# Kernel optimization log

Hardware: AMD Instinct MI355X
Metric: run time of the kernel (lower is better)

The kernel has to match this reference:

```python
import jax, jax.numpy as jnp
import numpy as np

D_MODEL = 1024
NUM_HEADS = 16
D_K = D_MODEL // NUM_HEADS


def setup_inputs() -> dict:
    key = jax.random.key(0)
    ks = jax.random.split(key, 9)
    B, S = 4, 2048
    scale = 1.0 / np.sqrt(D_MODEL)
    x = jax.random.normal(ks[0], (B, S, D_MODEL), dtype=jnp.float32)
    wq = jax.random.normal(ks[1], (D_MODEL, D_MODEL), dtype=jnp.float32) * scale
    wk = jax.random.normal(ks[2], (D_MODEL, D_MODEL), dtype=jnp.float32) * scale
    wv = jax.random.normal(ks[3], (D_MODEL, D_MODEL), dtype=jnp.float32) * scale
    wo = jax.random.normal(ks[4], (D_MODEL, D_MODEL), dtype=jnp.float32) * scale
    bq = jax.random.normal(ks[5], (D_MODEL,), dtype=jnp.float32) * 0.01
    bk = jax.random.normal(ks[6], (D_MODEL,), dtype=jnp.float32) * 0.01
    bv = jax.random.normal(ks[7], (D_MODEL,), dtype=jnp.float32) * 0.01
    bo = jax.random.normal(ks[8], (D_MODEL,), dtype=jnp.float32) * 0.01
    return {"x": x, "wq": wq, "bq": bq, "wk": wk, "bk": bk,
            "wv": wv, "bv": bv, "wo": wo, "bo": bo}


def reference(x, wq, bq, wk, bk, wv, bv, wo, bo):
    B, S, _ = x.shape
    # projections -> [B, H, S, d_k]
    def split_heads(t):
        return t.reshape(B, S, NUM_HEADS, D_K).transpose(0, 2, 1, 3)
    q = split_heads(x @ wq.T + bq)
    k = split_heads(x @ wk.T + bk)
    v = split_heads(x @ wv.T + bv)
    scores = jnp.einsum("bhqd,bhkd->bhqk", q, k) / np.sqrt(D_K).astype(np.float32)
    attn = jax.nn.softmax(scores, axis=-1)  # dropout is identity at eval
    out = jnp.einsum("bhqk,bhkd->bhqd", attn, v)
    out = out.transpose(0, 2, 1, 3).reshape(B, S, D_MODEL)
    return out @ wo.T + bo
```

## Files before the change

kernel.cpp:

```cpp
#include <hip/hip_runtime.h>

#define D_MODEL 1024
#define NHEADS  16
#define DK      64
#define BATCH   4
#define SEQ     2048
#define MROWS   (BATCH*SEQ)
#define BHCOUNT (BATCH*NHEADS)
#define KTILES  (SEQ/64)

typedef _Float16 half8 __attribute__((ext_vector_type(8)));
typedef _Float16 half4 __attribute__((ext_vector_type(4)));
typedef float    floatx4 __attribute__((ext_vector_type(4)));
typedef float    floatx16 __attribute__((ext_vector_type(16)));

__device__ __forceinline__ void load_lds16(const void* g, void* l) {
    __builtin_amdgcn_global_load_lds((const __attribute__((address_space(1))) void*)g,
                                     (__attribute__((address_space(3))) void*)l, 16, 0, 0);
}

__device__ __forceinline__ unsigned pkrtz_u32(float a, float b) {
    auto h = __builtin_amdgcn_cvt_pkrtz(a, b);
    union { decltype(h) v; unsigned u; } c; c.v = h; return c.u;
}

__device__ __forceinline__ int permrow(int r) {
    return (r & ~12) | ((r & 4) << 1) | ((r & 8) >> 1);
}

__global__ __launch_bounds__(256)
void cvt_f32_f16(const float* __restrict__ in, _Float16* __restrict__ out) {
    size_t i = ((size_t)blockIdx.x*256 + threadIdx.x)*4;
    float4 v = *(const float4*)(in + i);
    half4 h = {(_Float16)v.x, (_Float16)v.y, (_Float16)v.z, (_Float16)v.w};
    *(half4*)(out + i) = h;
}

__global__ __launch_bounds__(256)
void cvt4_f32_f16(const float* __restrict__ a, const float* __restrict__ b,
                  const float* __restrict__ c, const float* __restrict__ d,
                  _Float16* __restrict__ oa, _Float16* __restrict__ ob,
                  _Float16* __restrict__ oc, _Float16* __restrict__ od) {
    const float* src; _Float16* dst;
    switch (blockIdx.y) {
        case 0:  src=a; dst=oa; break;
        case 1:  src=b; dst=ob; break;
        case 2:  src=c; dst=oc; break;
        default: src=d; dst=od; break;
    }
    size_t i = ((size_t)blockIdx.x*256 + threadIdx.x)*4;
    float4 v = *(const float4*)(src + i);
    half4 h = {(_Float16)v.x, (_Float16)v.y, (_Float16)v.z, (_Float16)v.w};
    *(half4*)(dst + i) = h;
}

template<int MODE>
__global__ __launch_bounds__(256)
void gemm_nt_f16(const _Float16* __restrict__ A, const _Float16* __restrict__ W,
                 const float* __restrict__ bias, void* __restrict__ Cout, float scale)
{
    __shared__ _Float16 As[2][128*64];
    __shared__ _Float16 Ws[2][128*64];
    const int t = threadIdx.x;
    const int w = t >> 6, l = t & 63;
    const int wm = w >> 1, wn = w & 1;

    const int L   = blockIdx.x + (int)gridDim.x * blockIdx.y;
    const int cpx = (int)(gridDim.x * gridDim.y) >> 3;
    const int wid = (L & 7) * cpx + (L >> 3);
    const int bn  = (wid & 7) * 128;
    const int bm  = (wid >> 3) * 128;

    const int lrow = l & 15, lq4 = l >> 4;

    int srow[4], scol[4];
    #pragma unroll
    for (int it = 0; it < 4; ++it) {
        int s = (it*4 + w)*64 + l;
        int r = s >> 3;
        srow[it] = r;
        scol[it] = ((s & 7) ^ (r & 7))*8;
    }

    floatx4 acc[4][4];
    #pragma unroll
    for (int i = 0; i < 4; ++i)
        #pragma unroll
        for (int j = 0; j < 4; ++j) acc[i][j] = (floatx4){0.f,0.f,0.f,0.f};

    #pragma unroll
    for (int it = 0; it < 4; ++it) {
        load_lds16(A + (size_t)(bm + srow[it])*1024 + scol[it], &As[0][((it*4+w)*64+l)*8]);
        load_lds16(W + (size_t)(bn + srow[it])*1024 + scol[it], &Ws[0][((it*4+w)*64+l)*8]);
    }

    for (int kt = 0; kt < 16; ++kt) {
        __syncthreads();
        const int cur = kt & 1;
        if (kt + 1 < 16) {
            const int k1 = (kt + 1)*64;
            #pragma unroll
            for (int it = 0; it < 4; ++it) {
                load_lds16(A + (size_t)(bm + srow[it])*1024 + k1 + scol[it], &As[cur^1][((it*4+w)*64+l)*8]);
                load_lds16(W + (size_t)(bn + srow[it])*1024 + k1 + scol[it], &Ws[cur^1][((it*4+w)*64+l)*8]);
            }
        }
        #pragma unroll
        for (int ks = 0; ks < 2; ++ks) {
            const int xg = (((ks*4) ^ lq4 ^ (lrow & 7)))*8;
            half8 af[4], bf[4];
            #pragma unroll
            for (int i = 0; i < 4; ++i) af[i] = *(half8*)&As[cur][(wm*64 + i*16 + lrow)*64 + xg];
            #pragma unroll
            for (int j = 0; j < 4; ++j) bf[j] = *(half8*)&Ws[cur][(wn*64 + j*16 + lrow)*64 + xg];
            __builtin_amdgcn_s_setprio(1);
            #pragma unroll
            for (int i = 0; i < 4; ++i)
                #pragma unroll
                for (int j = 0; j < 4; ++j)
                    acc[i][j] = __builtin_amdgcn_mfma_f32_16x16x32_f16(af[i], bf[j], acc[i][j], 0, 0, 0);
            __builtin_amdgcn_s_setprio(0);
        }
    }

    #pragma unroll
    for (int j = 0; j < 4; ++j) {
        int gcol = bn + wn*64 + j*16 + lrow;
        float bv = bias[gcol];
        #pragma unroll
        for (int i = 0; i < 4; ++i) {
            #pragma unroll
            for (int r = 0; r < 4; ++r) {
                int gm = bm + wm*64 + i*16 + lq4*4 + r;
                float val = (acc[i][j][r] + bv) * scale;
                if (MODE == 0) {
                    ((float*)Cout)[(size_t)gm*1024 + gcol] = val;
                } else {
                    int b = gm >> 11, s = gm & 2047;
                    int h = gcol >> 6, dk = gcol & 63;
                    ((_Float16*)Cout)[(((size_t)(b*NHEADS + h))*SEQ + s)*DK + dk] = (_Float16)val;
                }
            }
        }
    }
}

__global__ __launch_bounds__(256)
void transpose_v(const _Float16* __restrict__ V, _Float16* __restrict__ Vt)
{
    __shared__ unsigned Lt[64][33];
    const int t = threadIdx.x;
    const int bh = blockIdx.y;
    const int s0 = blockIdx.x*64;
    const _Float16* Vb = V + ((size_t)bh*SEQ + s0)*DK;
    const int sp = t >> 3, dkc = (t & 7)*8;
    uint4 r0 = *(const uint4*)(Vb + (2*sp+0)*64 + dkc);
    uint4 r1 = *(const uint4*)(Vb + (2*sp+1)*64 + dkc);
    unsigned a0[4] = {r0.x, r0.y, r0.z, r0.w};
    unsigned a1[4] = {r1.x, r1.y, r1.z, r1.w};
    #pragma unroll
    for (int i = 0; i < 4; ++i) {
        Lt[dkc+2*i+0][sp] = (a0[i] & 0xFFFFu) | (a1[i] << 16);
        Lt[dkc+2*i+1][sp] = (a0[i] >> 16)     | (a1[i] & 0xFFFF0000u);
    }
    __syncthreads();
    const int dk = t >> 2, spc = (t & 3)*8;
    uint4 o0 = {Lt[dk][spc+0], Lt[dk][spc+1], Lt[dk][spc+2], Lt[dk][spc+3]};
    uint4 o1 = {Lt[dk][spc+4], Lt[dk][spc+5], Lt[dk][spc+6], Lt[dk][spc+7]};
    _Float16* dst = Vt + ((size_t)bh*DK + dk)*SEQ + s0 + spc*2;
    *(uint4*)(dst)     = o0;
    *(uint4*)(dst + 8) = o1;
}

__global__ __launch_bounds__(128)
void attn_mfma(const _Float16* __restrict__ Q, const _Float16* __restrict__ K,
               const _Float16* __restrict__ Vt, _Float16* __restrict__ AO)
{
    __shared__ _Float16 Ks[2][64*64];
    __shared__ _Float16 Vs[2][64*64];

    const int t = threadIdx.x;
    const int w = t >> 6, l = t & 63;
    const int l31 = l & 31, hi = l >> 5;

    const int L   = blockIdx.x + (int)gridDim.x * blockIdx.y;
    const int wid = (L & 7) * 128 + (L >> 3);
    const int bh  = wid >> 4;
    const int q0  = (wid & 15) * 128;

    const _Float16* Qb = Q  + ((size_t)bh*SEQ + q0)*DK;
    const _Float16* Kb = K  + (size_t)bh*SEQ*DK;
    const _Float16* Vb = Vt + (size_t)bh*DK*SEQ;

    int srow[4], scol[4], karow[4];
    #pragma unroll
    for (int it = 0; it < 4; ++it) {
        int s = (it*2 + w)*64 + l;
        int r = s >> 3;
        int lc = (s & 7) ^ (r & 7);
        srow[it] = r; scol[it] = lc*8;
        karow[it] = permrow(r);
    }

    half8 qf[2][4];
    #pragma unroll
    for (int qt = 0; qt < 2; ++qt)
        #pragma unroll
        for (int kk = 0; kk < 4; ++kk)
            qf[qt][kk] = *(const half8*)(Qb + (size_t)(w*64 + qt*32 + l31)*DK + kk*16 + hi*8);

    #pragma unroll
    for (int it = 0; it < 4; ++it) {
        load_lds16(Kb + (size_t)karow[it]*DK + scol[it], &Ks[0][(it*2+w)*512]);
        load_lds16(Vb + (size_t)srow[it]*SEQ + scol[it], &Vs[0][(it*2+w)*512]);
    }

    floatx16 Oacc[2][2];
    floatx16 lacc[2];
    #pragma unroll
    for (int qt = 0; qt < 2; ++qt) {
        #pragma unroll
        for (int i = 0; i < 16; ++i) { Oacc[qt][0][i] = 0.f; Oacc[qt][1][i] = 0.f; lacc[qt][i] = 0.f; }
    }
    floatx16 z16;
    #pragma unroll
    for (int i = 0; i < 16; ++i) z16[i] = 0.f;
    half8 onesf;
    #pragma unroll
    for (int i = 0; i < 8; ++i) onesf[i] = (_Float16)1.f;

#define ATTN_PREFETCH(NBUF, KT1)                                                          \
    if ((KT1) < KTILES) {                                                                 \
        _Pragma("unroll")                                                                 \
        for (int it = 0; it < 4; ++it) {                                                  \
            load_lds16(Kb + ((size_t)((KT1)*64 + karow[it]))*DK + scol[it],               \
                       &Ks[NBUF][(it*2+w)*512]);                                          \
            load_lds16(Vb + (size_t)srow[it]*SEQ + (KT1)*64 + scol[it],                   \
                       &Vs[NBUF][(it*2+w)*512]);                                          \
        }                                                                                 \
    }

#define ATTN_STEP(CUR, KT)                                                                \
    {                                                                                     \
        __syncthreads();                                                                  \
        ATTN_PREFETCH((CUR)^1, (KT)+1)                                                    \
        _Pragma("unroll")                                                                 \
        for (int kb = 0; kb < 2; ++kb) {                                                  \
            const int row = kb*32 + l31;                                                  \
                                \
            floatx16 sTa, sTb;                                                            \
            {                                                                             \
                half8 kf = *(half8*)&Ks[CUR][row*64 + ((hi ^ (row & 7)))*8];              \
                sTa = __builtin_amdgcn_mfma_f32_32x32x16_f16(kf, qf[0][0], z16, 0, 0, 0); \
                sTb = __builtin_amdgcn_mfma_f32_32x32x16_f16(kf, qf[1][0], z16, 0, 0, 0); \
            }                                                                             \
            _Pragma("unroll")                                                             \
            for (int kk = 1; kk < 4; ++kk) {                                              \
                half8 kf = *(half8*)&Ks[CUR][row*64 + (((kk*2 + hi) ^ (row & 7)))*8];     \
                sTa = __builtin_amdgcn_mfma_f32_32x32x16_f16(kf, qf[0][kk], sTa, 0, 0, 0);\
                sTb = __builtin_amdgcn_mfma_f32_32x32x16_f16(kf, qf[1][kk], sTb, 0, 0, 0);\
            }                                                                             \
                     \
            unsigned Wda[8], Wdb[8];                                                      \
            _Pragma("unroll")                                                             \
            for (int p = 0; p < 8; ++p) {                                                 \
                Wda[p] = pkrtz_u32(__builtin_amdgcn_exp2f(sTa[2*p]),                      \
                                   __builtin_amdgcn_exp2f(sTa[2*p+1]));                   \
                Wdb[p] = pkrtz_u32(__builtin_amdgcn_exp2f(sTb[2*p]),                      \
                                   __builtin_amdgcn_exp2f(sTb[2*p+1]));                   \
            }                                                                             \
                                     \
            _Pragma("unroll")                                                             \
            for (int kk2 = 0; kk2 < 2; ++kk2) {                                           \
                union { unsigned u[4]; half8 h; } pfa, pfb;                               \
                _Pragma("unroll")                                                         \
                for (int v = 0; v < 4; ++v) { pfa.u[v] = Wda[kk2*4 + v];                  \
                                              pfb.u[v] = Wdb[kk2*4 + v]; }                \
                lacc[0] = __builtin_amdgcn_mfma_f32_32x32x16_f16(pfa.h, onesf, lacc[0], 0, 0, 0); \
                lacc[1] = __builtin_amdgcn_mfma_f32_32x32x16_f16(pfb.h, onesf, lacc[1], 0, 0, 0); \
                const int vg = kb*4 + kk2*2 + hi;                                         \
                _Pragma("unroll")                                                         \
                for (int n = 0; n < 2; ++n) {                                             \
                    const int vrow = n*32 + l31;                                          \
                    half8 vf = *(half8*)&Vs[CUR][vrow*64 + ((vg ^ (vrow & 7)))*8];        \
                    Oacc[0][n] = __builtin_amdgcn_mfma_f32_32x32x16_f16(pfa.h, vf, Oacc[0][n], 0, 0, 0); \
                    Oacc[1][n] = __builtin_amdgcn_mfma_f32_32x32x16_f16(pfb.h, vf, Oacc[1][n], 0, 0, 0); \
                }                                                                         \
            }                                                                             \
        }                                                                                 \
    }

    for (int ktp = 0; ktp < KTILES; ktp += 2) {
        ATTN_STEP(0, ktp)
        ATTN_STEP(1, ktp+1)
    }
#undef ATTN_STEP
#undef ATTN_PREFETCH

    const int b = bh >> 4, h = bh & 15;
    #pragma unroll
    for (int qt = 0; qt < 2; ++qt)
        #pragma unroll
        for (int r = 0; r < 16; ++r) {
            float inv = 1.f / lacc[qt][r];
            int qrow = (r & 3) + 8*(r >> 2) + 4*hi;
            int gq = q0 + w*64 + qt*32 + qrow;
            _Float16* dst = AO + ((size_t)(b*SEQ + gq))*D_MODEL + h*DK;
            dst[l31]      = (_Float16)(Oacc[qt][0][r] * inv);
            dst[32 + l31] = (_Float16)(Oacc[qt][1][r] * inv);
        }
}

extern "C" void kernel_launch(void* const* d_in, const int* in_sizes, int n_in,
                              void* d_out, int out_size, void* d_ws, size_t ws_size,
                              hipStream_t stream)
{
    const float* x  = (const float*)d_in[0];
    const float* wq = (const float*)d_in[1];
    const float* bq = (const float*)d_in[2];
    const float* wk = (const float*)d_in[3];
    const float* bk = (const float*)d_in[4];
    const float* wv = (const float*)d_in[5];
    const float* bv = (const float*)d_in[6];
    const float* wo = (const float*)d_in[7];
    const float* bo = (const float*)d_in[8];

    const size_t NX = (size_t)MROWS * D_MODEL;
    const size_t NW = (size_t)D_MODEL * D_MODEL;
    _Float16* xh  = (_Float16*)d_ws;
    _Float16* wqh = xh  + NX;
    _Float16* wkh = wqh + NW;
    _Float16* wvh = wkh + NW;
    _Float16* woh = wvh + NW;
    _Float16* Qh  = woh + NW;
    _Float16* Kh  = Qh  + NX;
    _Float16* Vh  = Kh  + NX;
    _Float16* Vth = Vh  + NX;
    _Float16* AOh = Vth + NX;

    cvt_f32_f16<<<NX/1024, 256, 0, stream>>>(x, xh);
    cvt4_f32_f16<<<dim3(NW/1024, 4), 256, 0, stream>>>(wq, wk, wv, wo, wqh, wkh, wvh, woh);

    const float QSCALE = 0.125f * 1.44269504f;
    dim3 pgrid(D_MODEL/128, MROWS/128);
    gemm_nt_f16<1><<<pgrid, 256, 0, stream>>>(xh, wqh, bq, Qh, QSCALE);
    gemm_nt_f16<1><<<pgrid, 256, 0, stream>>>(xh, wkh, bk, Kh, 1.0f);
    gemm_nt_f16<1><<<pgrid, 256, 0, stream>>>(xh, wvh, bv, Vh, 1.0f);

    transpose_v<<<dim3(SEQ/64, BHCOUNT), 256, 0, stream>>>(Vh, Vth);
    attn_mfma<<<dim3(SEQ/128, BHCOUNT), 128, 0, stream>>>(Qh, Kh, Vth, AOh);

    gemm_nt_f16<0><<<pgrid, 256, 0, stream>>>(AOh, woh, bo, d_out, 1.0f);
}
```

Measured before the change: 299.4 us.

## Fuse Q/K/V projections into one GEMM launch with BK=32 tiles

The three separate Q, K and V projection GEMMs become a single launch over a 3x wider N grid. Contiguous wq/wk/wv half buffers act as one 3072x1024 weight, and each tile picks its bias, scale and output buffer from its column block. The GEMM is templated on the K tile depth with a matching LDS swizzle, and the fused launch uses BK=32 to halve shared memory per block and allow more resident blocks. The aim is to cut launch overhead and tail effects across three small grids, at the cost of more K iterations and barriers per tile.

New measurement: 300.0 us. No clear change (+0.2%).

```diff
diff --git a/kernel.cpp b/kernel.cpp
--- a/kernel.cpp
+++ b/kernel.cpp
@@ -54,32 +54,39 @@
     *(half4*)(dst + i) = h;
 }
 
-template<int MODE>
+template<int MODE, int BK>
 __global__ __launch_bounds__(256)
 void gemm_nt_f16(const _Float16* __restrict__ A, const _Float16* __restrict__ W,
-                 const float* __restrict__ bias, void* __restrict__ Cout, float scale)
+                 const float* __restrict__ b0, const float* __restrict__ b1,
+                 const float* __restrict__ b2, void* __restrict__ Cout, float qscale)
 {
-    __shared__ _Float16 As[2][128*64];
-    __shared__ _Float16 Ws[2][128*64];
+    constexpr int GR  = BK/8;
+    constexpr int NIT = BK/16;
+    constexpr int NKT = 1024/BK;
+    constexpr int KS  = BK/32;
+    __shared__ _Float16 As[2][128*BK];
+    __shared__ _Float16 Ws[2][128*BK];
     const int t = threadIdx.x;
     const int w = t >> 6, l = t & 63;
     const int wm = w >> 1, wn = w & 1;
 
     const int L   = blockIdx.x + (int)gridDim.x * blockIdx.y;
+    const int nbx = gridDim.x;
     const int cpx = (int)(gridDim.x * gridDim.y) >> 3;
     const int wid = (L & 7) * cpx + (L >> 3);
-    const int bn  = (wid & 7) * 128;
-    const int bm  = (wid >> 3) * 128;
+    const int bn  = (wid % nbx) * 128;
+    const int bm  = (wid / nbx) * 128;
 
     const int lrow = l & 15, lq4 = l >> 4;
 
-    int srow[4], scol[4];
-    #pragma unroll
-    for (int it = 0; it < 4; ++it) {
+    int srow[NIT], scol[NIT];
+    #pragma unroll
+    for (int it = 0; it < NIT; ++it) {
         int s = (it*4 + w)*64 + l;
-        int r = s >> 3;
-        srow[it] = r;
-        scol[it] = ((s & 7) ^ (r & 7))*8;
+        int r = s / GR, g = s % GR, gs;
+        if constexpr (BK == 64) gs = g ^ (r & 7);
+        else                    gs = g ^ ((r >> 1) & 3);
+        srow[it] = r; scol[it] = gs*8;
     }
 
     floatx4 acc[4][4];
@@ -89,30 +96,32 @@
         for (int j = 0; j < 4; ++j) acc[i][j] = (floatx4){0.f,0.f,0.f,0.f};
 
     #pragma unroll
-    for (int it = 0; it < 4; ++it) {
-        load_lds16(A + (size_t)(bm + srow[it])*1024 + scol[it], &As[0][((it*4+w)*64+l)*8]);
-        load_lds16(W + (size_t)(bn + srow[it])*1024 + scol[it], &Ws[0][((it*4+w)*64+l)*8]);
-    }
-
-    for (int kt = 0; kt < 16; ++kt) {
+    for (int it = 0; it < NIT; ++it) {
+        load_lds16(A + (size_t)(bm + srow[it])*1024 + scol[it], &As[0][(it*4+w)*512]);
+        load_lds16(W + (size_t)(bn + srow[it])*1024 + scol[it], &Ws[0][(it*4+w)*512]);
+    }
+
+    for (int kt = 0; kt < NKT; ++kt) {
         __syncthreads();
         const int cur = kt & 1;
-        if (kt + 1 < 16) {
-            const int k1 = (kt + 1)*64;
-            #pragma unroll
-            for (int it = 0; it < 4; ++it) {
-                load_lds16(A + (size_t)(bm + srow[it])*1024 + k1 + scol[it], &As[cur^1][((it*4+w)*64+l)*8]);
-                load_lds16(W + (size_t)(bn + srow[it])*1024 + k1 + scol[it], &Ws[cur^1][((it*4+w)*64+l)*8]);
+        if (kt + 1 < NKT) {
+            const int k1 = (kt + 1)*BK;
+            #pragma unroll
+            for (int it = 0; it < NIT; ++it) {
+                load_lds16(A + (size_t)(bm + srow[it])*1024 + k1 + scol[it], &As[cur^1][(it*4+w)*512]);
+                load_lds16(W + (size_t)(bn + srow[it])*1024 + k1 + scol[it], &Ws[cur^1][(it*4+w)*512]);
             }
         }
         #pragma unroll
-        for (int ks = 0; ks < 2; ++ks) {
-            const int xg = (((ks*4) ^ lq4 ^ (lrow & 7)))*8;
+        for (int ks = 0; ks < KS; ++ks) {
+            int xg;
+            if constexpr (BK == 64) xg = ((ks*4 + lq4) ^ (lrow & 7))*8;
+            else                    xg = (lq4 ^ ((lrow >> 1) & 3))*8;
             half8 af[4], bf[4];
             #pragma unroll
-            for (int i = 0; i < 4; ++i) af[i] = *(half8*)&As[cur][(wm*64 + i*16 + lrow)*64 + xg];
-            #pragma unroll
-            for (int j = 0; j < 4; ++j) bf[j] = *(half8*)&Ws[cur][(wn*64 + j*16 + lrow)*64 + xg];
+            for (int i = 0; i < 4; ++i) af[i] = *(half8*)&As[cur][(wm*64 + i*16 + lrow)*BK + xg];
+            #pragma unroll
+            for (int j = 0; j < 4; ++j) bf[j] = *(half8*)&Ws[cur][(wn*64 + j*16 + lrow)*BK + xg];
             __builtin_amdgcn_s_setprio(1);
             #pragma unroll
             for (int i = 0; i < 4; ++i)
@@ -123,10 +132,14 @@
         }
     }
 
+    constexpr size_t NXc = (size_t)MROWS * D_MODEL;
+    const int which = bn >> 10;
+    const float* bptr = (which == 0) ? b0 : (which == 1) ? b1 : b2;
+    const float scale = (which == 0) ? qscale : 1.0f;
     #pragma unroll
     for (int j = 0; j < 4; ++j) {
         int gcol = bn + wn*64 + j*16 + lrow;
-        float bv = bias[gcol];
+        float bv = bptr[gcol & 1023];
         #pragma unroll
         for (int i = 0; i < 4; ++i) {
             #pragma unroll
@@ -136,9 +149,10 @@
                 if (MODE == 0) {
                     ((float*)Cout)[(size_t)gm*1024 + gcol] = val;
                 } else {
+                    int hc = gcol & 1023;
                     int b = gm >> 11, s = gm & 2047;
-                    int h = gcol >> 6, dk = gcol & 63;
-                    ((_Float16*)Cout)[(((size_t)(b*NHEADS + h))*SEQ + s)*DK + dk] = (_Float16)val;
+                    int h = hc >> 6, dk = hc & 63;
+                    ((_Float16*)Cout)[which*NXc + (((size_t)(b*NHEADS + h))*SEQ + s)*DK + dk] = (_Float16)val;
                 }
             }
         }
@@ -342,13 +356,13 @@
     cvt4_f32_f16<<<dim3(NW/1024, 4), 256, 0, stream>>>(wq, wk, wv, wo, wqh, wkh, wvh, woh);
 
     const float QSCALE = 0.125f * 1.44269504f;
-    dim3 pgrid(D_MODEL/128, MROWS/128);
-    gemm_nt_f16<1><<<pgrid, 256, 0, stream>>>(xh, wqh, bq, Qh, QSCALE);
-    gemm_nt_f16<1><<<pgrid, 256, 0, stream>>>(xh, wkh, bk, Kh, 1.0f);
-    gemm_nt_f16<1><<<pgrid, 256, 0, stream>>>(xh, wvh, bv, Vh, 1.0f);
+
+    gemm_nt_f16<1,32><<<dim3(3*D_MODEL/128, MROWS/128), 256, 0, stream>>>(
+        xh, wqh, bq, bk, bv, Qh, QSCALE);
 
     transpose_v<<<dim3(SEQ/64, BHCOUNT), 256, 0, stream>>>(Vh, Vth);
     attn_mfma<<<dim3(SEQ/128, BHCOUNT), 128, 0, stream>>>(Qh, Kh, Vth, AOh);
 
-    gemm_nt_f16<0><<<pgrid, 256, 0, stream>>>(AOh, woh, bo, d_out, 1.0f);
-}
+    gemm_nt_f16<0,64><<<dim3(D_MODEL/128, MROWS/128), 256, 0, stream>>>(
+        AOh, woh, bo, bo, bo, d_out, 1.0f);
+}
```
